# Kernel tuning notes

Measured on AMD Instinct MI355X. Metric: run time of the kernel, lower is better.

## Reference

```python
import jax, jax.numpy as jnp
import numpy as np

B, A, C, M = 16, 76725, 8, 32
EPS = 1e-4


def _iou(b1, b2):
    # b1: [A,4], b2: [M,4]; +1 pixel convention as in the torch source
    lt = jnp.maximum(b1[:, None, :2], b2[None, :, :2])
    rb = jnp.minimum(b1[:, None, 2:], b2[None, :, 2:])
    wh = jnp.clip(rb - lt + 1.0, 0.0)
    inter = wh[..., 0] * wh[..., 1]
    a1 = (b1[:, 2] - b1[:, 0] + 1.0) * (b1[:, 3] - b1[:, 1] + 1.0)
    a2 = (b2[:, 2] - b2[:, 0] + 1.0) * (b2[:, 3] - b2[:, 1] + 1.0)
    return inter / (a1[:, None] + a2[None, :] - inter)


def setup_inputs() -> dict:
    key = jax.random.key(0)
    k1, k2, k3, k4, k5, k6, k7, k8, k9 = jax.random.split(key, 9)
    # anchors: one shared set of boxes, tiled over batch (as RetinaNet does)
    acx = jax.random.uniform(k1, (A,)) * 480.0 + 16.0
    acy = jax.random.uniform(k2, (A,)) * 480.0 + 16.0
    aw = jax.random.uniform(k3, (A,)) * 96.0 + 16.0
    ah = jax.random.uniform(k4, (A,)) * 96.0 + 16.0
    anchor = jnp.stack([acx - 0.5 * aw, acy - 0.5 * ah, acx + 0.5 * aw, acy + 0.5 * ah], -1)
    anchors = jnp.tile(anchor[None], (B, 1, 1))
    # annotations: [B,M,5] = (x1,y1,x2,y2,label); last 8 per image padded with label -1
    x1 = jax.random.uniform(k5, (B, M)) * 380.0
    y1 = jax.random.uniform(k6, (B, M)) * 380.0
    w = jax.random.uniform(k7, (B, M)) * 80.0 + 20.0
    h = jax.random.uniform(k8, (B, M)) * 80.0 + 20.0
    lab = jax.random.randint(k9, (B, M), 0, C).astype(jnp.float32)
    lab = jnp.where(jnp.arange(M)[None, :] < M - 8, lab, -1.0)
    annotations = jnp.stack([x1, y1, x1 + w, y1 + h, lab], -1)
    kc, kr = jax.random.split(jax.random.fold_in(key, 7))
    classifications = jax.random.uniform(kc, (B, A, C), dtype=jnp.float32)
    regressions = jax.random.normal(kr, (B, A, 4), dtype=jnp.float32) * 0.1
    return {
        "classifications": classifications,
        "regressions": regressions,
        "anchors": anchors,
        "annotations": annotations,
    }


def reference(classifications, regressions, anchors, annotations):
    ALPHA, GAMMA = 0.25, 2.0
    dt = classifications.dtype
    nclass = classifications.shape[-1]
    # anchor geometry taken from anchors[0] (as in the torch source)
    anchor0 = anchors[0]
    aw = anchor0[:, 2] - anchor0[:, 0]
    ah = anchor0[:, 3] - anchor0[:, 1]
    acx = anchor0[:, 0] + 0.5 * aw
    acy = anchor0[:, 1] + 0.5 * ah
    norm = jnp.array([0.1, 0.1, 0.2, 0.2], dt)

    def per_image(cls_, reg, anch, ann):
        valid = ann[:, 4] > -0.5  # label != -1
        num_valid = valid.sum()
        iou = _iou(anch, ann[:, :4])  # [A,M]
        iou = jnp.where(valid[None, :], iou, -1.0)  # mask padded annotations
        iou_max = iou.max(axis=1)
        iou_arg = iou.argmax(axis=1)
        p = jnp.clip(cls_, EPS, 1.0 - EPS)  # [A,C]
        assigned = ann[iou_arg]  # [A,5] gather of best annotation per anchor
        pos = iou_max >= 0.4
        npos = pos.sum()
        one_hot = jax.nn.one_hot(assigned[:, 4].astype(jnp.int32), nclass, dtype=dt)
        # targets: -1 ignore, 0 negative (IoU<0.3), one-hot positive (IoU>=0.4)
        targets = jnp.where(pos[:, None], one_hot,
                            jnp.where((iou_max < 0.3)[:, None], 0.0, -1.0))
        is_one = targets == 1.0
        alpha_factor = jnp.where(is_one, ALPHA, 1.0 - ALPHA)
        focal_w = alpha_factor * jnp.where(is_one, 1.0 - p, p) ** GAMMA
        bce = -(targets * jnp.log(p) + (1.0 - targets) * jnp.log1p(-p))
        cls_loss = jnp.where(targets != -1.0, focal_w * bce, 0.0).sum() \
            / jnp.maximum(npos.astype(dt), 1.0)
        w0 = assigned[:, 2] - assigned[:, 0]
        h0 = assigned[:, 3] - assigned[:, 1]
        gcx = assigned[:, 0] + 0.5 * w0
        gcy = assigned[:, 1] + 0.5 * h0
        gw = jnp.clip(w0, 1.0)
        gh = jnp.clip(h0, 1.0)
        t = jnp.stack([(gcx - acx) / aw, (gcy - acy) / ah,
                       jnp.log(gw / aw), jnp.log(gh / ah)], -1) / norm  # [A,4]
        diff = jnp.abs(t - reg)
        sl1 = jnp.where(diff <= 1.0 / 9.0, 0.5 * 9.0 * diff ** 2, diff - 0.5 / 9.0)
        reg_sum = jnp.where(pos[:, None], sl1, 0.0).sum()
        reg_loss = jnp.where(npos > 0,
                             reg_sum / jnp.maximum(npos * 4, 1).astype(dt), 0.0)
        cls_loss = jnp.where(num_valid > 0, cls_loss, 0.0)
        reg_loss = jnp.where(num_valid > 0, reg_loss, 0.0)
        return cls_loss, reg_loss

    cl, rl = jax.vmap(per_image)(classifications, regressions, anchors, annotations)
    return jnp.mean(cl, keepdims=True), jnp.mean(rl, keepdims=True)
```

## Files before the change

### kernel.cpp

```cpp
#include <hip/hip_runtime.h>

#define NB 16
#define NA 76725
#define NC 8
#define NM 32
#define FEPS 1e-4f
#define APT 2
#define TPB 256
#define ANCH_PER_BLK (APT * TPB)
#define NBLK_X ((NA + ANCH_PER_BLK - 1) / ANCH_PER_BLK)

#define WS_ACC 0
#define WS_NVP (NB * 16)
#define WS_CNT (WS_NVP + 16)
#define WS_REC (WS_CNT + 16)
#define WS_EPI (WS_REC + NB * NM * 8)

__global__ __launch_bounds__(64) void focal_prep(
    const float* __restrict__ ann_, float* __restrict__ ws)
{
    const int b = blockIdx.x;
    const int m = threadIdx.x;
    if (m < 16) ws[WS_ACC + b * 16 + m] = 0.f;
    bool valid = false;
    float x1 = 0.f, y1 = 0.f, x2 = 0.f, y2 = 0.f, lab = -1.f;
    if (m < NM) {
        const float* r = ann_ + ((size_t)b * NM + m) * 5;
        x1 = r[0]; y1 = r[1]; x2 = r[2]; y2 = r[3]; lab = r[4];
        valid = lab > -0.5f;
        float* rec = ws + WS_REC + ((size_t)b * NM + m) * 8;
        rec[0] = 3e18f; rec[1] = 3e18f; rec[2] = -3e18f; rec[3] = -3e18f;
        rec[4] = 1.0f;  rec[5] = -1.f;  rec[6] = 0.f;    rec[7] = 0.f;
        reinterpret_cast<float4*>(ws + WS_EPI)[b * NM + m] = make_float4(0.f, 0.f, 0.f, 0.f);
    }
    const unsigned long long mask = __ballot(valid);
    const int cnt = __popcll(mask);
    __syncthreads();
    if (valid) {
        const int idx = __popcll(mask & ((1ull << m) - 1ull));
        float* rec = ws + WS_REC + ((size_t)b * NM + idx) * 8;
        rec[0] = x1; rec[1] = y1; rec[2] = x2 + 1.f; rec[3] = y2 + 1.f;
        rec[4] = (x2 - x1 + 1.f) * (y2 - y1 + 1.f);
        rec[5] = lab;
        const float w0 = x2 - x1, h0 = y2 - y1;
        reinterpret_cast<float4*>(ws + WS_EPI)[b * NM + idx] =
            make_float4(x1 + 0.5f * w0, y1 + 0.5f * h0,
                        __logf(fmaxf(w0, 1.f)), __logf(fmaxf(h0, 1.f)));
    }
    if (m == 0) {
        ws[WS_CNT + b] = (float)cnt;
        ws[WS_NVP + b] = (float)((cnt + 7) & ~7);
    }
}

__global__ __launch_bounds__(TPB, 4) void focal_main(
    const float* __restrict__ cls_,
    const float* __restrict__ reg_,
    const float* __restrict__ anch_,
    const float* __restrict__ tab,
    float* __restrict__ acc)
{
    const int b   = blockIdx.y;
    const int tid = threadIdx.x;

    __shared__ float  s_x1[NM], s_y1[NM], s_x21[NM], s_y21[NM], s_a2[NM], s_lab[NM];
    __shared__ float4 s_epi[NM];
    if (tid < NM) {
        const float4 r0 = reinterpret_cast<const float4*>(tab + WS_REC)[(b * NM + tid) * 2];
        const float4 r1 = reinterpret_cast<const float4*>(tab + WS_REC)[(b * NM + tid) * 2 + 1];
        s_x1[tid] = r0.x; s_y1[tid] = r0.y; s_x21[tid] = r0.z; s_y21[tid] = r0.w;
        s_a2[tid] = r1.x; s_lab[tid] = r1.y;
        s_epi[tid] = reinterpret_cast<const float4*>(tab + WS_EPI)[b * NM + tid];
    }
    int nvp = (int)tab[WS_NVP + b];
    nvp = __builtin_amdgcn_readfirstlane(nvp);
    __syncthreads();

    const int a0 = blockIdx.x * ANCH_PER_BLK + tid;

    bool   amask[APT];
    float4 an[APT], rg[APT], cv0[APT], cv1[APT];
    #pragma unroll
    for (int k = 0; k < APT; ++k) {
        const int a = a0 + k * TPB;
        amask[k] = (a < NA);
        const int ac = amask[k] ? a : (NA - 1);
        const size_t base = (size_t)b * NA + ac;
        an[k]  = reinterpret_cast<const float4*>(anch_)[base];
        rg[k]  = reinterpret_cast<const float4*>(reg_)[base];
        cv0[k] = reinterpret_cast<const float4*>(cls_)[base * 2];
        cv1[k] = reinterpret_cast<const float4*>(cls_)[base * 2 + 1];
    }
    __builtin_amdgcn_sched_barrier(0);

    float ax[APT], ay[APT], az1[APT], aw1[APT], area1[APT];
    float ib[APT], ub[APT];
    int   arg[APT];
    #pragma unroll
    for (int k = 0; k < APT; ++k) {
        ax[k]  = an[k].x; ay[k] = an[k].y;
        az1[k] = an[k].z + 1.f; aw1[k] = an[k].w + 1.f;
        area1[k] = (an[k].z - ax[k] + 1.f) * (an[k].w - ay[k] + 1.f);
        ib[k] = 0.f; ub[k] = 1.f; arg[k] = 0;
    }

    #pragma unroll 4
    for (int m = 0; m < nvp; ++m) {
        const float x1 = s_x1[m], y1 = s_y1[m];
        const float x21 = s_x21[m], y21 = s_y21[m];
        const float a2 = s_a2[m];
        #pragma unroll
        for (int k = 0; k < APT; ++k) {
            const float w = fminf(az1[k], x21) - fmaxf(ax[k], x1);
            const float h = fminf(aw1[k], y21) - fmaxf(ay[k], y1);
            const float inter = fmaxf(w, 0.f) * fmaxf(h, 0.f);
            const float u = area1[k] + a2 - inter;
            const bool better = inter * ub[k] > ib[k] * u;
            ib[k]  = better ? inter : ib[k];
            ub[k]  = better ? u : ub[k];
            arg[k] = better ? m : arg[k];
        }
    }

    float cls_c = 0.f, reg_c = 0.f;
    unsigned pos_c = 0;

    #pragma unroll
    for (int k = 0; k < APT; ++k) {
        const bool pos = ib[k] >= 0.4f * ub[k];
        const bool neg = ib[k] <  0.3f * ub[k];
        const bool act = (pos || neg) && amask[k];

        float pcl[8];
        {
            const float pv[8] = {cv0[k].x, cv0[k].y, cv0[k].z, cv0[k].w,
                                 cv1[k].x, cv1[k].y, cv1[k].z, cv1[k].w};
            float bsum = 0.f;
            #pragma unroll
            for (int c = 0; c < NC; ++c) {
                const float p = fminf(fmaxf(pv[c], FEPS), 1.f - FEPS);
                pcl[c] = p;
                bsum += 0.75f * p * p * (-__logf(1.f - p));
            }
            float contrib = bsum;
            if (pos) {
                const int labi = (int)s_lab[arg[k]];
                const float t0 = (labi & 1) ? pcl[1] : pcl[0];
                const float t1 = (labi & 1) ? pcl[3] : pcl[2];
                const float t2 = (labi & 1) ? pcl[5] : pcl[4];
                const float t3 = (labi & 1) ? pcl[7] : pcl[6];
                const float u0 = (labi & 2) ? t1 : t0;
                const float u1 = (labi & 2) ? t3 : t2;
                const float pt = (labi & 4) ? u1 : u0;
                const float om = 1.f - pt;
                contrib += 0.25f * om * om * (-__logf(pt))
                         - 0.75f * pt * pt * (-__logf(om));
            }
            cls_c += act ? contrib : 0.f;
        }

        if (pos && amask[k]) {
            pos_c += 1;
            const float4 ep = s_epi[arg[k]];
            const float awd = az1[k] - 1.f - ax[k];
            const float ahd = aw1[k] - 1.f - ay[k];
            const float acx = ax[k] + 0.5f * awd;
            const float acy = ay[k] + 0.5f * ahd;
            const float t0 = __fdividef(ep.x - acx, awd) * 10.f;
            const float t1 = __fdividef(ep.y - acy, ahd) * 10.f;
            const float t2 = (ep.z - __logf(awd)) * 5.f;
            const float t3 = (ep.w - __logf(ahd)) * 5.f;
            const float d0 = fabsf(t0 - rg[k].x);
            const float d1 = fabsf(t1 - rg[k].y);
            const float d2 = fabsf(t2 - rg[k].z);
            const float d3 = fabsf(t3 - rg[k].w);
            auto sl1 = [](float d) {
                return d <= (1.f / 9.f) ? 4.5f * d * d : d - (0.5f / 9.f);
            };
            reg_c += sl1(d0) + sl1(d1) + sl1(d2) + sl1(d3);
        }
    }

    #pragma unroll
    for (int off = 32; off > 0; off >>= 1) {
        cls_c += __shfl_down(cls_c, off);
        reg_c += __shfl_down(reg_c, off);
        pos_c += __shfl_down(pos_c, off);
    }
    __shared__ float    sc[4], sr[4];
    __shared__ unsigned sp[4];
    const int wave = tid >> 6, lane = tid & 63;
    if (lane == 0) { sc[wave] = cls_c; sr[wave] = reg_c; sp[wave] = pos_c; }
    __syncthreads();
    if (tid == 0) {
        const float    c = sc[0] + sc[1] + sc[2] + sc[3];
        const float    r = sr[0] + sr[1] + sr[2] + sr[3];
        const unsigned p = sp[0] + sp[1] + sp[2] + sp[3];
        atomicAdd(&acc[WS_ACC + b * 16 + 0], c);
        atomicAdd(&acc[WS_ACC + b * 16 + 1], r);
        atomicAdd(reinterpret_cast<unsigned*>(acc) + WS_ACC + b * 16 + 2, p);
    }
}

__global__ __launch_bounds__(64) void focal_finalize(
    const float* __restrict__ ws, float* __restrict__ out)
{
    __shared__ float s_cls[NB], s_reg[NB];
    const int b = threadIdx.x;
    if (b < NB) {
        const float    nv      = ws[WS_CNT + b];
        const float    cls_sum = ws[WS_ACC + b * 16 + 0];
        const float    reg_sum = ws[WS_ACC + b * 16 + 1];
        const unsigned npos    = reinterpret_cast<const unsigned*>(ws)[WS_ACC + b * 16 + 2];
        float cl = cls_sum / fmaxf((float)npos, 1.f);
        float rl = (npos > 0u) ? reg_sum / (float)(npos * 4u) : 0.f;
        if (nv < 0.5f) { cl = 0.f; rl = 0.f; }
        s_cls[b] = cl;
        s_reg[b] = rl;
    }
    __syncthreads();
    if (threadIdx.x == 0) {
        float c = 0.f, r = 0.f;
        for (int i = 0; i < NB; ++i) { c += s_cls[i]; r += s_reg[i]; }
        out[0] = c * (1.f / NB);
        out[1] = r * (1.f / NB);
    }
}

extern "C" void kernel_launch(void* const* d_in, const int* in_sizes, int n_in,
                              void* d_out, int out_size, void* d_ws, size_t ws_size,
                              hipStream_t stream)
{
    const float* cls_  = (const float*)d_in[0];
    const float* reg_  = (const float*)d_in[1];
    const float* anch_ = (const float*)d_in[2];
    const float* ann_  = (const float*)d_in[3];
    float* ws  = (float*)d_ws;
    float* out = (float*)d_out;

    focal_prep<<<NB, 64, 0, stream>>>(ann_, ws);
    dim3 grid(NBLK_X, NB);
    focal_main<<<grid, dim3(TPB), 0, stream>>>(cls_, reg_, anch_, ws, ws);
    focal_finalize<<<1, 64, 0, stream>>>(ws, out);
}
```

Measured before the change: 45.42 us.

## Use one anchor per thread with split IoU argmax chains over boxes

Each thread now handles one anchor instead of two, which doubles the grid size. Inside the IoU loop it runs two independent argmax accumulators over even and odd boxes, then merges them with a tie-break on the lower index. Box coordinates are packed into a float4 in shared memory so they load in one read, and the anchor load is issued before the table setup barrier. The aim is more parallelism and shorter dependency chains per thread, at the cost of more blocks, more per-block overhead and more atomics.

```diff
diff --git a/kernel.cpp b/kernel.cpp
--- a/kernel.cpp
+++ b/kernel.cpp
@@ -5,10 +5,8 @@
 #define NC 8
 #define NM 32
 #define FEPS 1e-4f
-#define APT 2
 #define TPB 256
-#define ANCH_PER_BLK (APT * TPB)
-#define NBLK_X ((NA + ANCH_PER_BLK - 1) / ANCH_PER_BLK)
+#define NBLK_X ((NA + TPB - 1) / TPB)
 
 #define WS_ACC 0
 #define WS_NVP (NB * 16)
@@ -63,12 +61,19 @@
     const int b   = blockIdx.y;
     const int tid = threadIdx.x;
 
-    __shared__ float  s_x1[NM], s_y1[NM], s_x21[NM], s_y21[NM], s_a2[NM], s_lab[NM];
+    const int a = blockIdx.x * TPB + tid;
+    const bool amask = (a < NA);
+    const size_t base = (size_t)b * NA + (amask ? a : (NA - 1));
+
+    const float4 an = reinterpret_cast<const float4*>(anch_)[base];
+
+    __shared__ float4 s_box[NM];
+    __shared__ float  s_a2[NM], s_lab[NM];
     __shared__ float4 s_epi[NM];
     if (tid < NM) {
         const float4 r0 = reinterpret_cast<const float4*>(tab + WS_REC)[(b * NM + tid) * 2];
         const float4 r1 = reinterpret_cast<const float4*>(tab + WS_REC)[(b * NM + tid) * 2 + 1];
-        s_x1[tid] = r0.x; s_y1[tid] = r0.y; s_x21[tid] = r0.z; s_y21[tid] = r0.w;
+        s_box[tid] = r0;
         s_a2[tid] = r1.x; s_lab[tid] = r1.y;
         s_epi[tid] = reinterpret_cast<const float4*>(tab + WS_EPI)[b * NM + tid];
     }
@@ -76,109 +81,106 @@
     nvp = __builtin_amdgcn_readfirstlane(nvp);
     __syncthreads();
 
-    const int a0 = blockIdx.x * ANCH_PER_BLK + tid;
-
-    bool   amask[APT];
-    float4 an[APT], rg[APT], cv0[APT], cv1[APT];
-    #pragma unroll
-    for (int k = 0; k < APT; ++k) {
-        const int a = a0 + k * TPB;
-        amask[k] = (a < NA);
-        const int ac = amask[k] ? a : (NA - 1);
-        const size_t base = (size_t)b * NA + ac;
-        an[k]  = reinterpret_cast<const float4*>(anch_)[base];
-        rg[k]  = reinterpret_cast<const float4*>(reg_)[base];
-        cv0[k] = reinterpret_cast<const float4*>(cls_)[base * 2];
-        cv1[k] = reinterpret_cast<const float4*>(cls_)[base * 2 + 1];
-    }
+    const float4 rg  = reinterpret_cast<const float4*>(reg_)[base];
+    const float4 cv0 = reinterpret_cast<const float4*>(cls_)[base * 2];
+    const float4 cv1 = reinterpret_cast<const float4*>(cls_)[base * 2 + 1];
     __builtin_amdgcn_sched_barrier(0);
 
-    float ax[APT], ay[APT], az1[APT], aw1[APT], area1[APT];
-    float ib[APT], ub[APT];
-    int   arg[APT];
-    #pragma unroll
-    for (int k = 0; k < APT; ++k) {
-        ax[k]  = an[k].x; ay[k] = an[k].y;
-        az1[k] = an[k].z + 1.f; aw1[k] = an[k].w + 1.f;
-        area1[k] = (an[k].z - ax[k] + 1.f) * (an[k].w - ay[k] + 1.f);
-        ib[k] = 0.f; ub[k] = 1.f; arg[k] = 0;
-    }
+    const float ax = an.x, ay = an.y;
+    const float az1 = an.z + 1.f, aw1 = an.w + 1.f;
+    const float area1 = (an.z - ax + 1.f) * (an.w - ay + 1.f);
+
+    float ib0 = 0.f, ub0 = 1.f, ib1 = 0.f, ub1 = 1.f;
+    int   arg0 = 0, arg1 = 0;
 
     #pragma unroll 4
-    for (int m = 0; m < nvp; ++m) {
-        const float x1 = s_x1[m], y1 = s_y1[m];
-        const float x21 = s_x21[m], y21 = s_y21[m];
-        const float a2 = s_a2[m];
-        #pragma unroll
-        for (int k = 0; k < APT; ++k) {
-            const float w = fminf(az1[k], x21) - fmaxf(ax[k], x1);
-            const float h = fminf(aw1[k], y21) - fmaxf(ay[k], y1);
+    for (int m = 0; m < nvp; m += 2) {
+        const float4 q0 = s_box[m];
+        const float  a20 = s_a2[m];
+        const float4 q1 = s_box[m + 1];
+        const float  a21 = s_a2[m + 1];
+        {
+            const float w = fminf(az1, q0.z) - fmaxf(ax, q0.x);
+            const float h = fminf(aw1, q0.w) - fmaxf(ay, q0.y);
             const float inter = fmaxf(w, 0.f) * fmaxf(h, 0.f);
-            const float u = area1[k] + a2 - inter;
-            const bool better = inter * ub[k] > ib[k] * u;
-            ib[k]  = better ? inter : ib[k];
-            ub[k]  = better ? u : ub[k];
-            arg[k] = better ? m : arg[k];
-        }
-    }
+            const float u = area1 + a20 - inter;
+            const bool better = inter * ub0 > ib0 * u;
+            ib0  = better ? inter : ib0;
+            ub0  = better ? u : ub0;
+            arg0 = better ? m : arg0;
+        }
+        {
+            const float w = fminf(az1, q1.z) - fmaxf(ax, q1.x);
+            const float h = fminf(aw1, q1.w) - fmaxf(ay, q1.y);
+            const float inter = fmaxf(w, 0.f) * fmaxf(h, 0.f);
+            const float u = area1 + a21 - inter;
+            const bool better = inter * ub1 > ib1 * u;
+            ib1  = better ? inter : ib1;
+            ub1  = better ? u : ub1;
+            arg1 = better ? m + 1 : arg1;
+        }
+    }
+
+    const float c0 = ib0 * ub1;
+    const float c1 = ib1 * ub0;
+    const bool take1 = (c1 > c0) || (c1 == c0 && arg1 < arg0);
+    const float ib = take1 ? ib1 : ib0;
+    const float ub = take1 ? ub1 : ub0;
+    const int   arg = take1 ? arg1 : arg0;
+
+    const bool pos = ib >= 0.4f * ub;
+    const bool neg = ib <  0.3f * ub;
+    const bool act = (pos || neg) && amask;
 
     float cls_c = 0.f, reg_c = 0.f;
     unsigned pos_c = 0;
 
-    #pragma unroll
-    for (int k = 0; k < APT; ++k) {
-        const bool pos = ib[k] >= 0.4f * ub[k];
-        const bool neg = ib[k] <  0.3f * ub[k];
-        const bool act = (pos || neg) && amask[k];
-
+    {
+        const float pv[8] = {cv0.x, cv0.y, cv0.z, cv0.w, cv1.x, cv1.y, cv1.z, cv1.w};
         float pcl[8];
-        {
-            const float pv[8] = {cv0[k].x, cv0[k].y, cv0[k].z, cv0[k].w,
-                                 cv1[k].x, cv1[k].y, cv1[k].z, cv1[k].w};
-            float bsum = 0.f;
-            #pragma unroll
-            for (int c = 0; c < NC; ++c) {
-                const float p = fminf(fmaxf(pv[c], FEPS), 1.f - FEPS);
-                pcl[c] = p;
-                bsum += 0.75f * p * p * (-__logf(1.f - p));
-            }
-            float contrib = bsum;
-            if (pos) {
-                const int labi = (int)s_lab[arg[k]];
-                const float t0 = (labi & 1) ? pcl[1] : pcl[0];
-                const float t1 = (labi & 1) ? pcl[3] : pcl[2];
-                const float t2 = (labi & 1) ? pcl[5] : pcl[4];
-                const float t3 = (labi & 1) ? pcl[7] : pcl[6];
-                const float u0 = (labi & 2) ? t1 : t0;
-                const float u1 = (labi & 2) ? t3 : t2;
-                const float pt = (labi & 4) ? u1 : u0;
-                const float om = 1.f - pt;
-                contrib += 0.25f * om * om * (-__logf(pt))
-                         - 0.75f * pt * pt * (-__logf(om));
-            }
-            cls_c += act ? contrib : 0.f;
-        }
-
-        if (pos && amask[k]) {
-            pos_c += 1;
-            const float4 ep = s_epi[arg[k]];
-            const float awd = az1[k] - 1.f - ax[k];
-            const float ahd = aw1[k] - 1.f - ay[k];
-            const float acx = ax[k] + 0.5f * awd;
-            const float acy = ay[k] + 0.5f * ahd;
-            const float t0 = __fdividef(ep.x - acx, awd) * 10.f;
-            const float t1 = __fdividef(ep.y - acy, ahd) * 10.f;
-            const float t2 = (ep.z - __logf(awd)) * 5.f;
-            const float t3 = (ep.w - __logf(ahd)) * 5.f;
-            const float d0 = fabsf(t0 - rg[k].x);
-            const float d1 = fabsf(t1 - rg[k].y);
-            const float d2 = fabsf(t2 - rg[k].z);
-            const float d3 = fabsf(t3 - rg[k].w);
-            auto sl1 = [](float d) {
-                return d <= (1.f / 9.f) ? 4.5f * d * d : d - (0.5f / 9.f);
-            };
-            reg_c += sl1(d0) + sl1(d1) + sl1(d2) + sl1(d3);
-        }
+        float bsum = 0.f;
+        #pragma unroll
+        for (int c = 0; c < NC; ++c) {
+            const float p = fminf(fmaxf(pv[c], FEPS), 1.f - FEPS);
+            pcl[c] = p;
+            bsum += 0.75f * p * p * (-__logf(1.f - p));
+        }
+        float contrib = bsum;
+        if (pos) {
+            const int labi = (int)s_lab[arg];
+            const float t0 = (labi & 1) ? pcl[1] : pcl[0];
+            const float t1 = (labi & 1) ? pcl[3] : pcl[2];
+            const float t2 = (labi & 1) ? pcl[5] : pcl[4];
+            const float t3 = (labi & 1) ? pcl[7] : pcl[6];
+            const float u0 = (labi & 2) ? t1 : t0;
+            const float u1 = (labi & 2) ? t3 : t2;
+            const float pt = (labi & 4) ? u1 : u0;
+            const float om = 1.f - pt;
+            contrib += 0.25f * om * om * (-__logf(pt))
+                     - 0.75f * pt * pt * (-__logf(om));
+        }
+        cls_c = act ? contrib : 0.f;
+    }
+
+    if (pos && amask) {
+        pos_c = 1;
+        const float4 ep = s_epi[arg];
+        const float awd = az1 - 1.f - ax;
+        const float ahd = aw1 - 1.f - ay;
+        const float acx = ax + 0.5f * awd;
+        const float acy = ay + 0.5f * ahd;
+        const float t0 = __fdividef(ep.x - acx, awd) * 10.f;
+        const float t1 = __fdividef(ep.y - acy, ahd) * 10.f;
+        const float t2 = (ep.z - __logf(awd)) * 5.f;
+        const float t3 = (ep.w - __logf(ahd)) * 5.f;
+        const float d0 = fabsf(t0 - rg.x);
+        const float d1 = fabsf(t1 - rg.y);
+        const float d2 = fabsf(t2 - rg.z);
+        const float d3 = fabsf(t3 - rg.w);
+        auto sl1 = [](float d) {
+            return d <= (1.f / 9.f) ? 4.5f * d * d : d - (0.5f / 9.f);
+        };
+        reg_c = sl1(d0) + sl1(d1) + sl1(d2) + sl1(d3);
     }
 
     #pragma unroll
```

Result: slower. 63.49 us (+39.8%).
